# Performance work log

Hardware: AMD Instinct MI355X
Metric: run time of the kernel (lower is better)

The kernel has to match this reference:

```python
import jax, jax.numpy as jnp
from jax import lax
import numpy as np

B = 131072   # batch
F = 512      # resnet18 pooled feature dim
D = 32       # latent_dim
T = 4        # pre-drawn rejection-sampling trials (accept always fires on trial 0 for d=32,k>=1)
H = 512      # MLP hidden
FS = 32      # MLP final_size
O = 7        # num_classes * action_length


def _normalize(x, eps=1e-12):
    # matches torch F.normalize: x / max(||x||, eps)
    n = jnp.linalg.norm(x, axis=-1, keepdims=True)
    return x / jnp.maximum(n, eps)


def setup_inputs() -> dict:
    key = jax.random.key(0)
    ks = jax.random.split(key, 16)
    s = 0.02
    return {
        "h": jax.random.normal(ks[0], (B, F), jnp.float32),
        "v": jax.random.normal(ks[1], (B, D), jnp.float32),
        "zu": jax.random.uniform(ks[2], (T, B), jnp.float32),
        "uu": jax.random.uniform(ks[3], (T, B), jnp.float32),
        "W_mu": jax.random.normal(ks[4], (F, D), jnp.float32) * s,
        "b_mu": jnp.zeros((D,), jnp.float32),
        "W_k": jax.random.normal(ks[5], (F, 1), jnp.float32) * s,
        "b_k": jnp.zeros((1,), jnp.float32),
        "W1": jax.random.normal(ks[6], (D, H), jnp.float32) * s,
        "b1": jnp.zeros((H,), jnp.float32),
        "W2": jax.random.normal(ks[7], (H, H), jnp.float32) * s,
        "b2": jnp.zeros((H,), jnp.float32),
        "W3": jax.random.normal(ks[8], (H, FS), jnp.float32) * s,
        "b3": jnp.zeros((FS,), jnp.float32),
        "W4": jax.random.normal(ks[9], (FS, O), jnp.float32) * s,
        "b4": jnp.zeros((O,), jnp.float32),
    }


def _sample_vmf_radial(k, zu, uu, d):
    """Vectorized accept-reject radial sampling. k:[B], zu/uu:[T,B] -> w:[B].
    First-accept semantics across the T pre-drawn trials (replaces the Python
    per-sample while loop; for this module the first trial always accepts)."""
    def step(carry, inp):
        w, done = carry
        z_raw, u = inp
        e = jnp.exp(-2.0 * k)
        z = z_raw * (1.0 - e) + e
        w_t = 1.0 - jnp.log(z) / k
        acc = jnp.log(u) <= (d - 3.0) * jnp.log(w_t) + k * w_t
        take = jnp.logical_and(acc, jnp.logical_not(done))
        return (jnp.where(take, w_t, w), jnp.logical_or(done, acc)), None
    (w, _), _ = lax.scan(step, (jnp.zeros_like(k), jnp.zeros(k.shape, bool)), (zu, uu))
    return w


def reference(h, v, zu, uu, W_mu, b_mu, W_k, b_k, W1, b1, W2, b2, W3, b3, W4, b4):
    # encode
    mu = _normalize(h @ W_mu + b_mu)                     # [B, D]
    kappa = jax.nn.softplus(h @ W_k + b_k) + 1.0         # [B, 1]
    # reparameterize
    k = kappa[:, 0]
    w = _sample_vmf_radial(k, zu, uu, float(D))          # [B]
    vn = _normalize(v)
    u_h = _normalize(vn - mu)
    z = vn - 2.0 * jnp.sum(vn * u_h, axis=-1, keepdims=True) * u_h  # Householder
    z = z * w[:, None]
    # MLP head
    x = jax.nn.relu(z @ W1 + b1)
    x = jax.nn.relu(x @ W2 + b2)
    x = jax.nn.relu(x @ W3 + b3)
    out = x @ W4 + b4                                    # [B, O]
    return (out, mu, kappa)
```

## Files before the change

### kernel.cpp

```cpp
#include <hip/hip_runtime.h>
#include <stdint.h>

#define B_N 131072

typedef float        float4_ __attribute__((ext_vector_type(4)));
typedef short        short8  __attribute__((ext_vector_type(8)));
typedef unsigned int uint4_  __attribute__((ext_vector_type(4)));

__device__ __forceinline__ unsigned short f2bf(float f) {
    unsigned int u = __float_as_uint(f);
    u += 0x7fffu + ((u >> 16) & 1u);
    return (unsigned short)(u >> 16);
}
__device__ __forceinline__ unsigned int pack2bf(float lo, float hi) {
    return (unsigned int)f2bf(lo) | ((unsigned int)f2bf(hi) << 16);
}

__global__ void aehr_prep(const float* __restrict__ Wmu, const float* __restrict__ Wk,
                          const float* __restrict__ W1, const float* __restrict__ W2,
                          const float* __restrict__ W3,
                          unsigned short* __restrict__ wct, unsigned short* __restrict__ w1t,
                          unsigned short* __restrict__ w2k, unsigned short* __restrict__ w3p) {
    int idx = blockIdx.x * 256 + threadIdx.x;
    if (idx < 48 * 512) {
        int n = idx >> 9, k = idx & 511;
        float v = 0.0f;
        if (n < 32) v = Wmu[k * 32 + n];
        else if (n == 32) v = Wk[k];
        wct[idx] = f2bf(v);
    } else if (idx < 48 * 512 + 512 * 32) {
        int j = idx - 48 * 512;
        int n = j >> 5, k = j & 31;
        w1t[j] = f2bf(W1[k * 512 + n]);
    } else if (idx < 48 * 512 + 512 * 32 + 512 * 512) {
        int j = idx - (48 * 512 + 512 * 32);
        int i = j & 7, t = j >> 3;
        int n = t & 511, gk = t >> 9;
        int g = gk & 3, ks = gk >> 2;
        int col = ks * 32 + ((i < 4) ? (4 * g + i) : (16 + 4 * g + (i - 4)));
        w2k[j] = f2bf(W2[col * 512 + n]);
    } else if (idx < 48 * 512 + 512 * 32 + 512 * 512 + 32 * 512) {
        int j = idx - (48 * 512 + 512 * 32 + 512 * 512);
        int n = j >> 9, slot = j & 511;
        int s = slot >> 5, q = slot & 31, g = (q >> 3) & 3, i = q & 7;
        int col = s * 32 + ((i < 4) ? (4 * g + i) : (16 + 4 * g + (i - 4)));
        w3p[j] = f2bf(W3[col * 32 + n]);
    }
}

__global__ __launch_bounds__(256, 4) void aehr_front(
    const float* __restrict__ h, const float* __restrict__ v,
    const float* __restrict__ zu, const float* __restrict__ uu,
    const float* __restrict__ bmu, const float* __restrict__ bk,
    const unsigned short* __restrict__ wct,
    float* __restrict__ out, unsigned short* __restrict__ zws)
{
    const int tid = threadIdx.x;
    const int wv = tid >> 6;
    const int ln = tid & 63;
    const int g = ln >> 4;
    const int c = ln & 15;
    const int rowA = blockIdx.x * 64 + wv * 16 + c;

    float4_ fz = {0.f, 0.f, 0.f, 0.f};
    float4_ acc0 = fz, acc1 = fz, acc2 = fz;
    const float* hrow = h + (size_t)rowA * 512 + g * 8;

    for (int ks = 0; ks < 16; ++ks) {
        float4_ a0 = *(const float4_*)(hrow + ks * 32);
        float4_ a1 = *(const float4_*)(hrow + ks * 32 + 4);
        short8 af;
        af[0] = (short)f2bf(a0[0]); af[1] = (short)f2bf(a0[1]);
        af[2] = (short)f2bf(a0[2]); af[3] = (short)f2bf(a0[3]);
        af[4] = (short)f2bf(a1[0]); af[5] = (short)f2bf(a1[1]);
        af[6] = (short)f2bf(a1[2]); af[7] = (short)f2bf(a1[3]);
        int kbase = ks * 32 + g * 8;
        short8 bf0 = *(const short8*)(wct + (c * 512 + kbase));
        short8 bf1 = *(const short8*)(wct + ((16 + c) * 512 + kbase));
        short8 bf2 = *(const short8*)(wct + ((32 + c) * 512 + kbase));
        acc0 = __builtin_amdgcn_mfma_f32_16x16x32_bf16(af, bf0, acc0, 0, 0, 0);
        acc1 = __builtin_amdgcn_mfma_f32_16x16x32_bf16(af, bf1, acc1, 0, 0, 0);
        acc2 = __builtin_amdgcn_mfma_f32_16x16x32_bf16(af, bf2, acc2, 0, 0, 0);
    }

    const float bm0 = bmu[c], bm1 = bmu[16 + c];
    const float bk0 = bk[0];

    #pragma unroll
    for (int r = 0; r < 4; ++r) {
        const int gm = blockIdx.x * 64 + wv * 16 + 4 * g + r;
        float m0 = acc0[r] + bm0;
        float m1 = acc1[r] + bm1;
        float s = m0 * m0 + m1 * m1;
        s += __shfl_xor(s, 1); s += __shfl_xor(s, 2);
        s += __shfl_xor(s, 4); s += __shfl_xor(s, 8);
        float nrm = fmaxf(sqrtf(s), 1e-12f);
        float mu0 = m0 / nrm, mu1 = m1 / nrm;
        out[(size_t)B_N * 7 + (size_t)gm * 32 + c] = mu0;
        out[(size_t)B_N * 7 + (size_t)gm * 32 + 16 + c] = mu1;

        float kraw = __shfl(acc2[r], g * 16) + bk0;
        float kap = fmaxf(kraw, 0.f) + log1pf(expf(-fabsf(kraw))) + 1.0f;
        if (c == 0) out[(size_t)B_N * 39 + gm] = kap;

        float e = expf(-2.0f * kap);
        float ome = 1.0f - e;
        float w = 0.0f;
        bool done = false;
        #pragma unroll
        for (int t = 0; t < 4; ++t) {
            float zr = zu[t * B_N + gm];
            float ur = uu[t * B_N + gm];
            float zt = zr * ome + e;
            float wt = 1.0f - logf(zt) / kap;
            bool ac = (logf(ur) <= 29.0f * logf(wt) + kap * wt);
            if (ac && !done) w = wt;
            done = done || ac;
        }

        float v0 = v[(size_t)gm * 32 + c];
        float v1 = v[(size_t)gm * 32 + 16 + c];
        float sv = v0 * v0 + v1 * v1;
        sv += __shfl_xor(sv, 1); sv += __shfl_xor(sv, 2);
        sv += __shfl_xor(sv, 4); sv += __shfl_xor(sv, 8);
        float vn = fmaxf(sqrtf(sv), 1e-12f);
        float vn0 = v0 / vn, vn1 = v1 / vn;

        float u0 = vn0 - mu0, u1 = vn1 - mu1;
        float su = u0 * u0 + u1 * u1;
        su += __shfl_xor(su, 1); su += __shfl_xor(su, 2);
        su += __shfl_xor(su, 4); su += __shfl_xor(su, 8);
        float un = fmaxf(sqrtf(su), 1e-12f);
        float uh0 = u0 / un, uh1 = u1 / un;

        float dt = vn0 * uh0 + vn1 * uh1;
        dt += __shfl_xor(dt, 1); dt += __shfl_xor(dt, 2);
        dt += __shfl_xor(dt, 4); dt += __shfl_xor(dt, 8);

        float z0 = (vn0 - 2.0f * dt * uh0) * w;
        float z1 = (vn1 - 2.0f * dt * uh1) * w;
        zws[(size_t)gm * 32 + c] = f2bf(z0);
        zws[(size_t)gm * 32 + 16 + c] = f2bf(z1);
    }
}

__global__ __launch_bounds__(512, 2) void aehr_mlp(
    const unsigned short* __restrict__ zws,
    const unsigned short* __restrict__ w1t,
    const unsigned short* __restrict__ w2k,
    const unsigned short* __restrict__ w3p,
    const float* __restrict__ b1, const float* __restrict__ b2,
    const float* __restrict__ b3, const float* __restrict__ W4,
    const float* __restrict__ b4,
    float* __restrict__ out)
{
    __shared__ __attribute__((aligned(16))) char smem[67584];
    const int tid = threadIdx.x;
    const int wv = tid >> 6;
    const int ln = tid & 63;
    const int g = ln >> 4;
    const int c = ln & 15;
    const int swz = (c & 7) << 4;
    const size_t rowbase = (size_t)blockIdx.x * 64;
    const float4_ fz = {0.f, 0.f, 0.f, 0.f};

    {
        short8 zf[4];
        #pragma unroll
        for (int rt = 0; rt < 4; ++rt)
            zf[rt] = *(const short8*)(zws + (rowbase + rt * 16 + c) * 32 + g * 8);

        #pragma unroll
        for (int sl = 0; sl < 2; ++sl) {
            const int nb0 = wv * 64 + sl * 32;
            short8 w1f0 = *(const short8*)(w1t + (nb0 + c) * 32 + g * 8);
            short8 w1f1 = *(const short8*)(w1t + (nb0 + 16 + c) * 32 + g * 8);
            float4_ bv0 = *(const float4_*)(b1 + nb0 + 4 * g);
            float4_ bv1 = *(const float4_*)(b1 + nb0 + 16 + 4 * g);
            const int S = wv * 2 + sl;
            #pragma unroll
            for (int rt = 0; rt < 4; ++rt) {
                float4_ d0 = __builtin_amdgcn_mfma_f32_16x16x32_bf16(w1f0, zf[rt], fz, 0, 0, 0);
                float4_ d1 = __builtin_amdgcn_mfma_f32_16x16x32_bf16(w1f1, zf[rt], fz, 0, 0, 0);
                uint4_ u;
                u[0] = pack2bf(fmaxf(d0[0] + bv0[0], 0.f), fmaxf(d0[1] + bv0[1], 0.f));
                u[1] = pack2bf(fmaxf(d0[2] + bv0[2], 0.f), fmaxf(d0[3] + bv0[3], 0.f));
                u[2] = pack2bf(fmaxf(d1[0] + bv1[0], 0.f), fmaxf(d1[1] + bv1[1], 0.f));
                u[3] = pack2bf(fmaxf(d1[2] + bv1[2], 0.f), fmaxf(d1[3] + bv1[3], 0.f));
                const int row = rt * 16 + c;
                *(uint4_*)(smem + row * 1024 + ((S * 64 + g * 16) ^ swz)) = u;
            }
        }
    }
    __syncthreads();

    float4_ acc[4][4];
    #pragma unroll
    for (int rt = 0; rt < 4; ++rt)
        #pragma unroll
        for (int nt = 0; nt < 4; ++nt) acc[rt][nt] = fz;

    #pragma unroll 2
    for (int ks = 0; ks < 16; ++ks) {
        const unsigned short* wb = w2k + (size_t)(ks * 4 + g) * 512 * 8 + (wv * 64 + c) * 8;
        short8 a[4];
        #pragma unroll
        for (int nt = 0; nt < 4; ++nt)
            a[nt] = *(const short8*)(wb + nt * 128);
        #pragma unroll
        for (int rt = 0; rt < 4; ++rt) {
            short8 bfr = *(const short8*)(smem + (rt * 16 + c) * 1024 + ((ks * 64 + g * 16) ^ swz));
            #pragma unroll
            for (int nt = 0; nt < 4; ++nt)
                acc[rt][nt] = __builtin_amdgcn_mfma_f32_16x16x32_bf16(a[nt], bfr, acc[rt][nt], 0, 0, 0);
        }
    }

    float4_ x3acc[4][2];
    #pragma unroll
    for (int rt = 0; rt < 4; ++rt) { x3acc[rt][0] = fz; x3acc[rt][1] = fz; }
    {
        short8 w3f[2][2];
        #pragma unroll
        for (int S = 0; S < 2; ++S)
            #pragma unroll
            for (int n3 = 0; n3 < 2; ++n3)
                w3f[S][n3] = *(const short8*)(w3p + (n3 * 16 + c) * 512 + (wv * 2 + S) * 32 + g * 8);

        float4_ bv0 = *(const float4_*)(b2 + wv * 64 + 4 * g);
        float4_ bv1 = *(const float4_*)(b2 + wv * 64 + 16 + 4 * g);
        float4_ bv2 = *(const float4_*)(b2 + wv * 64 + 32 + 4 * g);
        float4_ bv3 = *(const float4_*)(b2 + wv * 64 + 48 + 4 * g);

        #pragma unroll
        for (int rt = 0; rt < 4; ++rt) {
            union { uint4_ u; short8 s; } x2a, x2b;
            x2a.u[0] = pack2bf(fmaxf(acc[rt][0][0] + bv0[0], 0.f), fmaxf(acc[rt][0][1] + bv0[1], 0.f));
            x2a.u[1] = pack2bf(fmaxf(acc[rt][0][2] + bv0[2], 0.f), fmaxf(acc[rt][0][3] + bv0[3], 0.f));
            x2a.u[2] = pack2bf(fmaxf(acc[rt][1][0] + bv1[0], 0.f), fmaxf(acc[rt][1][1] + bv1[1], 0.f));
            x2a.u[3] = pack2bf(fmaxf(acc[rt][1][2] + bv1[2], 0.f), fmaxf(acc[rt][1][3] + bv1[3], 0.f));
            x2b.u[0] = pack2bf(fmaxf(acc[rt][2][0] + bv2[0], 0.f), fmaxf(acc[rt][2][1] + bv2[1], 0.f));
            x2b.u[1] = pack2bf(fmaxf(acc[rt][2][2] + bv2[2], 0.f), fmaxf(acc[rt][2][3] + bv2[3], 0.f));
            x2b.u[2] = pack2bf(fmaxf(acc[rt][3][0] + bv3[0], 0.f), fmaxf(acc[rt][3][1] + bv3[1], 0.f));
            x2b.u[3] = pack2bf(fmaxf(acc[rt][3][2] + bv3[2], 0.f), fmaxf(acc[rt][3][3] + bv3[3], 0.f));
            #pragma unroll
            for (int n3 = 0; n3 < 2; ++n3) {
                x3acc[rt][n3] = __builtin_amdgcn_mfma_f32_16x16x32_bf16(w3f[0][n3], x2a.s, x3acc[rt][n3], 0, 0, 0);
                x3acc[rt][n3] = __builtin_amdgcn_mfma_f32_16x16x32_bf16(w3f[1][n3], x2b.s, x3acc[rt][n3], 0, 0, 0);
            }
        }
    }
    __syncthreads();

    float* red = (float*)smem;
    #pragma unroll
    for (int rt = 0; rt < 4; ++rt)
        #pragma unroll
        for (int t3 = 0; t3 < 2; ++t3)
            #pragma unroll
            for (int r = 0; r < 4; ++r)
                red[wv * 2112 + (rt * 16 + c) * 33 + t3 * 16 + 4 * g + r] = x3acc[rt][t3][r];
    __syncthreads();

    float sums[4];
    #pragma unroll
    for (int k = 0; k < 4; ++k) {
        int idx = tid + k * 512;
        int row = idx >> 5, n = idx & 31;
        float s_ = b3[n];
        #pragma unroll
        for (int w_ = 0; w_ < 8; ++w_) s_ += red[w_ * 2112 + row * 33 + n];
        sums[k] = fmaxf(s_, 0.0f);
    }
    __syncthreads();

    float* x3f = (float*)smem;
    #pragma unroll
    for (int k = 0; k < 4; ++k) {
        int idx = tid + k * 512;
        x3f[(idx >> 5) * 33 + (idx & 31)] = sums[k];
    }
    __syncthreads();

    {
        const int row = tid >> 3;
        const int o = tid & 7;
        if (o < 7) {
            const size_t gm = rowbase + row;
            float acc4 = b4[o];
            #pragma unroll
            for (int ci = 0; ci < 32; ++ci)
                acc4 += x3f[row * 33 + ci] * W4[ci * 7 + o];
            out[gm * 7 + o] = acc4;
        }
    }
}

extern "C" void kernel_launch(void* const* d_in, const int* in_sizes, int n_in,
                              void* d_out, int out_size, void* d_ws, size_t ws_size,
                              hipStream_t stream) {
    const float* h   = (const float*)d_in[0];
    const float* v   = (const float*)d_in[1];
    const float* zu  = (const float*)d_in[2];
    const float* uu  = (const float*)d_in[3];
    const float* Wmu = (const float*)d_in[4];
    const float* bmu = (const float*)d_in[5];
    const float* Wk  = (const float*)d_in[6];
    const float* bk  = (const float*)d_in[7];
    const float* W1  = (const float*)d_in[8];
    const float* b1  = (const float*)d_in[9];
    const float* W2  = (const float*)d_in[10];
    const float* b2  = (const float*)d_in[11];
    const float* W3  = (const float*)d_in[12];
    const float* b3  = (const float*)d_in[13];
    const float* W4  = (const float*)d_in[14];
    const float* b4  = (const float*)d_in[15];

    float* out = (float*)d_out;
    char* ws = (char*)d_ws;
    unsigned short* zws = (unsigned short*)ws;
    unsigned short* wct = (unsigned short*)(ws + 8388608);
    unsigned short* w1t = (unsigned short*)(ws + 8437760);
    unsigned short* w2k = (unsigned short*)(ws + 8470528);
    unsigned short* w3p = (unsigned short*)(ws + 8994816);

    aehr_prep<<<1248, 256, 0, stream>>>(Wmu, Wk, W1, W2, W3, wct, w1t, w2k, w3p);
    aehr_front<<<2048, 256, 0, stream>>>(h, v, zu, uu, bmu, bk, wct, out, zws);
    aehr_mlp<<<2048, 512, 0, stream>>>(zws, w1t, w2k, w3p, b1, b2, b3, W4, b4, out);
}
```

Measured before the change: 177.0 us.

## Fuse encoder/reparam front kernel into MLP kernel via LDS-staged z

Merges the front kernel (h projection, kappa, vMF sampling, Householder) into the MLP kernel so z is kept in shared memory instead of being written to and reread from a global workspace. The fused kernel runs 256 threads per block (4 waves), so each wave now covers twice as many hidden columns in layers 1–3, processing W2 output in two passes. This removes one kernel launch and the z round trip through global memory. In exchange it reduces waves per block and occupancy (launch bounds 256,2), and the front-end's memory-bound h read is serialized with the MFMA-heavy MLP inside each block.

```diff
diff --git a/kernel.cpp b/kernel.cpp
--- a/kernel.cpp
+++ b/kernel.cpp
@@ -48,104 +48,11 @@
     }
 }
 
-__global__ __launch_bounds__(256, 4) void aehr_front(
+__global__ __launch_bounds__(256, 2) void aehr_fused(
     const float* __restrict__ h, const float* __restrict__ v,
     const float* __restrict__ zu, const float* __restrict__ uu,
     const float* __restrict__ bmu, const float* __restrict__ bk,
     const unsigned short* __restrict__ wct,
-    float* __restrict__ out, unsigned short* __restrict__ zws)
-{
-    const int tid = threadIdx.x;
-    const int wv = tid >> 6;
-    const int ln = tid & 63;
-    const int g = ln >> 4;
-    const int c = ln & 15;
-    const int rowA = blockIdx.x * 64 + wv * 16 + c;
-
-    float4_ fz = {0.f, 0.f, 0.f, 0.f};
-    float4_ acc0 = fz, acc1 = fz, acc2 = fz;
-    const float* hrow = h + (size_t)rowA * 512 + g * 8;
-
-    for (int ks = 0; ks < 16; ++ks) {
-        float4_ a0 = *(const float4_*)(hrow + ks * 32);
-        float4_ a1 = *(const float4_*)(hrow + ks * 32 + 4);
-        short8 af;
-        af[0] = (short)f2bf(a0[0]); af[1] = (short)f2bf(a0[1]);
-        af[2] = (short)f2bf(a0[2]); af[3] = (short)f2bf(a0[3]);
-        af[4] = (short)f2bf(a1[0]); af[5] = (short)f2bf(a1[1]);
-        af[6] = (short)f2bf(a1[2]); af[7] = (short)f2bf(a1[3]);
-        int kbase = ks * 32 + g * 8;
-        short8 bf0 = *(const short8*)(wct + (c * 512 + kbase));
-        short8 bf1 = *(const short8*)(wct + ((16 + c) * 512 + kbase));
-        short8 bf2 = *(const short8*)(wct + ((32 + c) * 512 + kbase));
-        acc0 = __builtin_amdgcn_mfma_f32_16x16x32_bf16(af, bf0, acc0, 0, 0, 0);
-        acc1 = __builtin_amdgcn_mfma_f32_16x16x32_bf16(af, bf1, acc1, 0, 0, 0);
-        acc2 = __builtin_amdgcn_mfma_f32_16x16x32_bf16(af, bf2, acc2, 0, 0, 0);
-    }
-
-    const float bm0 = bmu[c], bm1 = bmu[16 + c];
-    const float bk0 = bk[0];
-
-    #pragma unroll
-    for (int r = 0; r < 4; ++r) {
-        const int gm = blockIdx.x * 64 + wv * 16 + 4 * g + r;
-        float m0 = acc0[r] + bm0;
-        float m1 = acc1[r] + bm1;
-        float s = m0 * m0 + m1 * m1;
-        s += __shfl_xor(s, 1); s += __shfl_xor(s, 2);
-        s += __shfl_xor(s, 4); s += __shfl_xor(s, 8);
-        float nrm = fmaxf(sqrtf(s), 1e-12f);
-        float mu0 = m0 / nrm, mu1 = m1 / nrm;
-        out[(size_t)B_N * 7 + (size_t)gm * 32 + c] = mu0;
-        out[(size_t)B_N * 7 + (size_t)gm * 32 + 16 + c] = mu1;
-
-        float kraw = __shfl(acc2[r], g * 16) + bk0;
-        float kap = fmaxf(kraw, 0.f) + log1pf(expf(-fabsf(kraw))) + 1.0f;
-        if (c == 0) out[(size_t)B_N * 39 + gm] = kap;
-
-        float e = expf(-2.0f * kap);
-        float ome = 1.0f - e;
-        float w = 0.0f;
-        bool done = false;
-        #pragma unroll
-        for (int t = 0; t < 4; ++t) {
-            float zr = zu[t * B_N + gm];
-            float ur = uu[t * B_N + gm];
-            float zt = zr * ome + e;
-            float wt = 1.0f - logf(zt) / kap;
-            bool ac = (logf(ur) <= 29.0f * logf(wt) + kap * wt);
-            if (ac && !done) w = wt;
-            done = done || ac;
-        }
-
-        float v0 = v[(size_t)gm * 32 + c];
-        float v1 = v[(size_t)gm * 32 + 16 + c];
-        float sv = v0 * v0 + v1 * v1;
-        sv += __shfl_xor(sv, 1); sv += __shfl_xor(sv, 2);
-        sv += __shfl_xor(sv, 4); sv += __shfl_xor(sv, 8);
-        float vn = fmaxf(sqrtf(sv), 1e-12f);
-        float vn0 = v0 / vn, vn1 = v1 / vn;
-
-        float u0 = vn0 - mu0, u1 = vn1 - mu1;
-        float su = u0 * u0 + u1 * u1;
-        su += __shfl_xor(su, 1); su += __shfl_xor(su, 2);
-        su += __shfl_xor(su, 4); su += __shfl_xor(su, 8);
-        float un = fmaxf(sqrtf(su), 1e-12f);
-        float uh0 = u0 / un, uh1 = u1 / un;
-
-        float dt = vn0 * uh0 + vn1 * uh1;
-        dt += __shfl_xor(dt, 1); dt += __shfl_xor(dt, 2);
-        dt += __shfl_xor(dt, 4); dt += __shfl_xor(dt, 8);
-
-        float z0 = (vn0 - 2.0f * dt * uh0) * w;
-        float z1 = (vn1 - 2.0f * dt * uh1) * w;
-        zws[(size_t)gm * 32 + c] = f2bf(z0);
-        zws[(size_t)gm * 32 + 16 + c] = f2bf(z1);
-    }
-}
-
-__global__ __launch_bounds__(512, 2) void aehr_mlp(
-    const unsigned short* __restrict__ zws,
     const unsigned short* __restrict__ w1t,
     const unsigned short* __restrict__ w2k,
     const unsigned short* __restrict__ w3p,
@@ -154,7 +61,8 @@
     const float* __restrict__ b4,
     float* __restrict__ out)
 {
-    __shared__ __attribute__((aligned(16))) char smem[67584];
+    __shared__ __attribute__((aligned(16))) char smem[70656];
+    unsigned short* zl = (unsigned short*)(smem + 65536);
     const int tid = threadIdx.x;
     const int wv = tid >> 6;
     const int ln = tid & 63;
@@ -165,19 +73,104 @@
     const float4_ fz = {0.f, 0.f, 0.f, 0.f};
 
     {
+        float4_ acc0 = fz, acc1 = fz, acc2 = fz;
+        const int rowA = (int)rowbase + wv * 16 + c;
+        const float* hrow = h + (size_t)rowA * 512 + g * 8;
+
+        for (int ks = 0; ks < 16; ++ks) {
+            float4_ a0 = *(const float4_*)(hrow + ks * 32);
+            float4_ a1 = *(const float4_*)(hrow + ks * 32 + 4);
+            short8 af;
+            af[0] = (short)f2bf(a0[0]); af[1] = (short)f2bf(a0[1]);
+            af[2] = (short)f2bf(a0[2]); af[3] = (short)f2bf(a0[3]);
+            af[4] = (short)f2bf(a1[0]); af[5] = (short)f2bf(a1[1]);
+            af[6] = (short)f2bf(a1[2]); af[7] = (short)f2bf(a1[3]);
+            int kbase = ks * 32 + g * 8;
+            short8 bf0 = *(const short8*)(wct + (c * 512 + kbase));
+            short8 bf1 = *(const short8*)(wct + ((16 + c) * 512 + kbase));
+            short8 bf2 = *(const short8*)(wct + ((32 + c) * 512 + kbase));
+            acc0 = __builtin_amdgcn_mfma_f32_16x16x32_bf16(af, bf0, acc0, 0, 0, 0);
+            acc1 = __builtin_amdgcn_mfma_f32_16x16x32_bf16(af, bf1, acc1, 0, 0, 0);
+            acc2 = __builtin_amdgcn_mfma_f32_16x16x32_bf16(af, bf2, acc2, 0, 0, 0);
+        }
+
+        const float bm0 = bmu[c], bm1 = bmu[16 + c];
+        const float bk0 = bk[0];
+
+        #pragma unroll
+        for (int r = 0; r < 4; ++r) {
+            const int lrow = wv * 16 + 4 * g + r;
+            const int gm = (int)rowbase + lrow;
+            float m0 = acc0[r] + bm0;
+            float m1 = acc1[r] + bm1;
+            float s = m0 * m0 + m1 * m1;
+            s += __shfl_xor(s, 1); s += __shfl_xor(s, 2);
+            s += __shfl_xor(s, 4); s += __shfl_xor(s, 8);
+            float nrm = fmaxf(sqrtf(s), 1e-12f);
+            float mu0 = m0 / nrm, mu1 = m1 / nrm;
+            out[(size_t)B_N * 7 + (size_t)gm * 32 + c] = mu0;
+            out[(size_t)B_N * 7 + (size_t)gm * 32 + 16 + c] = mu1;
+
+            float kraw = __shfl(acc2[r], g * 16) + bk0;
+            float kap = fmaxf(kraw, 0.f) + log1pf(expf(-fabsf(kraw))) + 1.0f;
+            if (c == 0) out[(size_t)B_N * 39 + gm] = kap;
+
+            float e = expf(-2.0f * kap);
+            float ome = 1.0f - e;
+            float w = 0.0f;
+            bool done = false;
+            #pragma unroll
+            for (int t = 0; t < 4; ++t) {
+                float zr = zu[t * B_N + gm];
+                float ur = uu[t * B_N + gm];
+                float zt = zr * ome + e;
+                float wt = 1.0f - logf(zt) / kap;
+                bool ac = (logf(ur) <= 29.0f * logf(wt) + kap * wt);
+                if (ac && !done) w = wt;
+                done = done || ac;
+            }
+
+            float v0 = v[(size_t)gm * 32 + c];
+            float v1 = v[(size_t)gm * 32 + 16 + c];
+            float sv = v0 * v0 + v1 * v1;
+            sv += __shfl_xor(sv, 1); sv += __shfl_xor(sv, 2);
+            sv += __shfl_xor(sv, 4); sv += __shfl_xor(sv, 8);
+            float vn = fmaxf(sqrtf(sv), 1e-12f);
+            float vn0 = v0 / vn, vn1 = v1 / vn;
+
+            float u0 = vn0 - mu0, u1 = vn1 - mu1;
+            float su = u0 * u0 + u1 * u1;
+            su += __shfl_xor(su, 1); su += __shfl_xor(su, 2);
+            su += __shfl_xor(su, 4); su += __shfl_xor(su, 8);
+            float un = fmaxf(sqrtf(su), 1e-12f);
+            float uh0 = u0 / un, uh1 = u1 / un;
+
+            float dt = vn0 * uh0 + vn1 * uh1;
+            dt += __shfl_xor(dt, 1); dt += __shfl_xor(dt, 2);
+            dt += __shfl_xor(dt, 4); dt += __shfl_xor(dt, 8);
+
+            float z0 = (vn0 - 2.0f * dt * uh0) * w;
+            float z1 = (vn1 - 2.0f * dt * uh1) * w;
+            zl[lrow * 40 + c] = f2bf(z0);
+            zl[lrow * 40 + 16 + c] = f2bf(z1);
+        }
+    }
+    __syncthreads();
+
+    {
         short8 zf[4];
         #pragma unroll
         for (int rt = 0; rt < 4; ++rt)
-            zf[rt] = *(const short8*)(zws + (rowbase + rt * 16 + c) * 32 + g * 8);
-
-        #pragma unroll
-        for (int sl = 0; sl < 2; ++sl) {
-            const int nb0 = wv * 64 + sl * 32;
+            zf[rt] = *(const short8*)(zl + (rt * 16 + c) * 40 + g * 8);
+
+        #pragma unroll
+        for (int sl = 0; sl < 4; ++sl) {
+            const int nb0 = wv * 128 + sl * 32;
             short8 w1f0 = *(const short8*)(w1t + (nb0 + c) * 32 + g * 8);
             short8 w1f1 = *(const short8*)(w1t + (nb0 + 16 + c) * 32 + g * 8);
             float4_ bv0 = *(const float4_*)(b1 + nb0 + 4 * g);
             float4_ bv1 = *(const float4_*)(b1 + nb0 + 16 + 4 * g);
-            const int S = wv * 2 + sl;
+            const int S = wv * 4 + sl;
             #pragma unroll
             for (int rt = 0; rt < 4; ++rt) {
                 float4_ d0 = __builtin_amdgcn_mfma_f32_16x16x32_bf16(w1f0, zf[rt], fz, 0, 0, 0);
@@ -194,43 +187,47 @@
     }
     __syncthreads();
 
-    float4_ acc[4][4];
-    #pragma unroll
-    for (int rt = 0; rt < 4; ++rt)
-        #pragma unroll
-        for (int nt = 0; nt < 4; ++nt) acc[rt][nt] = fz;
-
-    #pragma unroll 2
-    for (int ks = 0; ks < 16; ++ks) {
-        const unsigned short* wb = w2k + (size_t)(ks * 4 + g) * 512 * 8 + (wv * 64 + c) * 8;
-        short8 a[4];
-        #pragma unroll
-        for (int nt = 0; nt < 4; ++nt)
-            a[nt] = *(const short8*)(wb + nt * 128);
-        #pragma unroll
-        for (int rt = 0; rt < 4; ++rt) {
-            short8 bfr = *(const short8*)(smem + (rt * 16 + c) * 1024 + ((ks * 64 + g * 16) ^ swz));
+    float4_ x3acc[4][2];
+    #pragma unroll
+    for (int rt = 0; rt < 4; ++rt) { x3acc[rt][0] = fz; x3acc[rt][1] = fz; }
+
+    #pragma unroll
+    for (int p = 0; p < 2; ++p) {
+        const int nb0 = wv * 128 + p * 64;
+        float4_ acc[4][4];
+        #pragma unroll
+        for (int rt = 0; rt < 4; ++rt)
+            #pragma unroll
+            for (int nt = 0; nt < 4; ++nt) acc[rt][nt] = fz;
+
+        #pragma unroll 2
+        for (int ks = 0; ks < 16; ++ks) {
+            const unsigned short* wb = w2k + ((size_t)(ks * 4 + g) * 512 + nb0 + c) * 8;
+            short8 a[4];
             #pragma unroll
             for (int nt = 0; nt < 4; ++nt)
-                acc[rt][nt] = __builtin_amdgcn_mfma_f32_16x16x32_bf16(a[nt], bfr, acc[rt][nt], 0, 0, 0);
-        }
-    }
-
-    float4_ x3acc[4][2];
-    #pragma unroll
-    for (int rt = 0; rt < 4; ++rt) { x3acc[rt][0] = fz; x3acc[rt][1] = fz; }
-    {
+                a[nt] = *(const short8*)(wb + nt * 128);
+            #pragma unroll
+            for (int rt = 0; rt < 4; ++rt) {
+                short8 bfr = *(const short8*)(smem + (rt * 16 + c) * 1024 + ((ks * 64 + g * 16) ^ swz));
+                #pragma unroll
+                for (int nt = 0; nt < 4; ++nt)
+                    acc[rt][nt] = __builtin_amdgcn_mfma_f32_16x16x32_bf16(a[nt], bfr, acc[rt][nt], 0, 0, 0);
+            }
+        }
+
+        const int S2 = wv * 4 + p * 2;
         short8 w3f[2][2];
         #pragma unroll
-        for (int S = 0; S < 2; ++S)
+        for (int h2 = 0; h2 < 2; ++h2)
             #pragma unroll
             for (int n3 = 0; n3 < 2; ++n3)
-                w3f[S][n3] = *(const short8*)(w3p + (n3 * 16 + c) * 512 + (wv * 2 + S) * 32 + g * 8);
-
-        float4_ bv0 = *(const float4_*)(b2 + wv * 64 + 4 * g);
-        float4_ bv1 = *(const float4_*)(b2 + wv * 64 + 16 + 4 * g);
-        float4_ bv2 = *(const float4_*)(b2 + wv * 64 + 32 + 4 * g);
-        float4_ bv3 = *(const float4_*)(b2 + wv * 64 + 48 + 4 * g);
+                w3f[h2][n3] = *(const short8*)(w3p + (n3 * 16 + c) * 512 + (S2 + h2) * 32 + g * 8);
+
+        float4_ bv0 = *(const float4_*)(b2 + nb0 + 4 * g);
+        float4_ bv1 = *(const float4_*)(b2 + nb0 + 16 + 4 * g);
+        float4_ bv2 = *(const float4_*)(b2 + nb0 + 32 + 4 * g);
+        float4_ bv3 = *(const float4_*)(b2 + nb0 + 48 + 4 * g);
 
         #pragma unroll
         for (int rt = 0; rt < 4; ++rt) {
@@ -262,28 +259,29 @@
                 red[wv * 2112 + (rt * 16 + c) * 33 + t3 * 16 + 4 * g + r] = x3acc[rt][t3][r];
     __syncthreads();
 
-    float sums[4];
-    #pragma unroll
-    for (int k = 0; k < 4; ++k) {
-        int idx = tid + k * 512;
+    float sums[8];
+    #pragma unroll
+    for (int k = 0; k < 8; ++k) {
+        int idx = tid + k * 256;
         int row = idx >> 5, n = idx & 31;
         float s_ = b3[n];
         #pragma unroll
-        for (int w_ = 0; w_ < 8; ++w_) s_ += red[w_ * 2112 + row * 33 + n];
+        for (int w_ = 0; w_ < 4; ++w_) s_ += red[w_ * 2112 + row * 33 + n];
         sums[k] = fmaxf(s_, 0.0f);
     }
     __syncthreads();
 
     float* x3f = (float*)smem;
     #pragma unroll
-    for (int k = 0; k < 4; ++k) {
-        int idx = tid + k * 512;
+    for (int k = 0; k < 8; ++k) {
+        int idx = tid + k * 256;
         x3f[(idx >> 5) * 33 + (idx & 31)] = sums[k];
     }
     __syncthreads();
 
-    {
-        const int row = tid >> 3;
+    #pragma unroll
+    for (int half = 0; half < 2; ++half) {
+        const int row = (tid >> 3) + half * 32;
         const int o = tid & 7;
         if (o < 7) {
             const size_t gm = rowbase + row;
@@ -318,13 +316,12 @@
 
     float* out = (float*)d_out;
     char* ws = (char*)d_ws;
-    unsigned short* zws = (unsigned short*)ws;
     unsigned short* wct = (unsigned short*)(ws + 8388608);
     unsigned short* w1t = (unsigned short*)(ws + 8437760);
     unsigned short* w2k = (unsigned short*)(ws + 8470528);
     unsigned short* w3p = (unsigned short*)(ws + 8994816);
 
     aehr_prep<<<1248, 256, 0, stream>>>(Wmu, Wk, W1, W2, W3, wct, w1t, w2k, w3p);
-    aehr_front<<<2048, 256, 0, stream>>>(h, v, zu, uu, bmu, bk, wct, out, zws);
-    aehr_mlp<<<2048, 512, 0, stream>>>(zws, w1t, w2k, w3p, b1, b2, b3, W4, b4, out);
-}
+    aehr_fused<<<2048, 256, 0, stream>>>(h, v, zu, uu, bmu, bk, wct, w1t, w2k, w3p,
+                                         b1, b2, b3, W4, b4, out);
+}
```

After: 195.4 us. 1.1x slower.
